# Optimization experiments

Measured on AMD Instinct MI355X. Metric: run time of the kernel, lower is better.

The kernel has to match this reference:

```python
import jax, jax.numpy as jnp
import numpy as np

LN_EPS = 1e-5
N_HEADS = 8

def _ln(x, g, b):
    mu = jnp.mean(x, axis=-1, keepdims=True)
    var = jnp.var(x, axis=-1, keepdims=True)
    return (x - mu) * jax.lax.rsqrt(var + LN_EPS) * g + b

def _glu(x):
    a, b = jnp.split(x, 2, axis=-1)
    return a * jax.nn.sigmoid(b)

def setup_inputs() -> dict:
    key = jax.random.key(0)
    ks = iter(jax.random.split(key, 48))
    B, C, HW, p = 16, 3, 224, 16
    d, N, M = 512, 2048, 25
    Sa, So, O, T = 512, 1024, 1000, 16
    P = (HW // p) ** 2
    rn = lambda shape, s=1.0: jax.random.normal(next(ks), shape, jnp.float32) * s
    inp = {
        'x': rn((B, C, HW, HW)),
        'conv_w': rn((d, C, p, p), 0.02), 'conv_b': jnp.zeros((d,)),
        'patch_ln_g': jnp.ones((d,)), 'patch_ln_b': jnp.zeros((d,)),
        'pos': rn((1, P, d), 0.02),
        'kv_w': rn((d, d), d ** -0.5), 'kv_b': jnp.zeros((d,)),
        'kv_ln_g': jnp.ones((d,)), 'kv_ln_b': jnp.zeros((d,)),
        'q_w': rn((d, Sa), Sa ** -0.5), 'q_b': jnp.zeros((d,)),
        'attn_in_w': rn((3 * d, d), d ** -0.5), 'attn_in_b': jnp.zeros((3 * d,)),
        'attn_out_w': rn((d, d), d ** -0.5), 'attn_out_b': jnp.zeros((d,)),
        'syn_w': rn((2 * N, d + N), (d + N) ** -0.5), 'syn_b': jnp.zeros((2 * N,)),
        'syn_ln_g': jnp.ones((N,)), 'syn_ln_b': jnp.zeros((N,)),
        'fc1_w': rn((N, M, 256), (2.0 / M) ** 0.5), 'fc1_b': jnp.zeros((N, 256)),
        'fc2_w': rn((N, 128, 2), (2.0 / 128) ** 0.5), 'fc2_b': jnp.zeros((N, 2)),
        'nlm_T': jnp.ones((1,)),
        'start_state': rn((N,), (1.0 / N) ** 0.5),
        'start_trace': rn((N, M), (1.0 / (N + M)) ** 0.5),
        'decay_action': jnp.zeros((Sa,)), 'decay_out': jnp.zeros((So,)),
        'out_w': rn((O, So), So ** -0.5), 'out_b': jnp.zeros((O,)),
        'act_left': jax.random.randint(next(ks), (Sa,), 0, N, jnp.int32),
        'act_right': jax.random.randint(next(ks), (Sa,), 0, N, jnp.int32),
        'out_left': jax.random.randint(next(ks), (So,), 0, N, jnp.int32),
        'out_right': jax.random.randint(next(ks), (So,), 0, N, jnp.int32),
        'ticks': T,
    }
    return inp

def _forward(x, conv_w, conv_b, patch_ln_g, patch_ln_b, pos, kv_w, kv_b, kv_ln_g, kv_ln_b,
             q_w, q_b, attn_in_w, attn_in_b, attn_out_w, attn_out_b,
             syn_w, syn_b, syn_ln_g, syn_ln_b, fc1_w, fc1_b, fc2_w, fc2_b, nlm_T,
             start_state, start_trace, decay_action, decay_out, out_w, out_b,
             act_left, act_right, out_left, out_right, ticks):
    B = x.shape[0]
    d = conv_w.shape[0]
    hd = d // N_HEADS
    scale = 1.0 / (hd ** 0.5)
    # --- patch embedding: Conv2d(stride=patch) -> flatten -> LN, then +pos ---
    pt = jax.lax.conv_general_dilated(
        x, conv_w, (conv_w.shape[2], conv_w.shape[3]), 'VALID',
        dimension_numbers=('NCHW', 'OIHW', 'NCHW')) + conv_b[None, :, None, None]
    pt = pt.reshape(B, d, -1).transpose(0, 2, 1)            # (B, P, d)
    pt = _ln(pt, patch_ln_g, patch_ln_b) + pos
    kv = _ln(pt @ kv_w.T + kv_b, kv_ln_g, kv_ln_b)          # (B, P, d)
    wq, wk, wv = jnp.split(attn_in_w, 3)
    bq, bk, bv = jnp.split(attn_in_b, 3)
    k = (kv @ wk.T + bk).reshape(B, -1, N_HEADS, hd)        # (B, P, H, hd)
    v = (kv @ wv.T + bv).reshape(B, -1, N_HEADS, hd)
    r_a = jnp.exp(-decay_action)
    r_o = jnp.exp(-decay_out)

    def sync(act, alpha, beta, r, left, right):
        pair = act[:, left] * act[:, right]                 # (B, S)
        alpha = r * alpha + pair
        beta = r * beta + 1.0
        return alpha * jax.lax.rsqrt(beta), alpha, beta

    def nlm(trace):
        h1 = _glu(jnp.einsum('bnm,nmh->bnh', trace, fc1_w) + fc1_b)  # (B, N, 128)
        h2 = _glu(jnp.einsum('bnh,nho->bno', h1, fc2_w) + fc2_b)     # (B, N, 1)
        return h2[..., 0] / nlm_T[0]

    act0 = jnp.broadcast_to(start_state, (B,) + start_state.shape)
    trace0 = jnp.broadcast_to(start_trace, (B,) + start_trace.shape)
    Sa = act_left.shape[0]
    So = out_left.shape[0]
    _, ao0, bo0 = sync(act0, jnp.zeros((B, So)), jnp.zeros((B, So)), r_o, out_left, out_right)
    carry0 = (trace0, act0, jnp.zeros((B, Sa)), jnp.zeros((B, Sa)), ao0, bo0)

    def step(carry, _):
        trace, act, aa, ba, ao, bo = carry
        s_act, aa, ba = sync(act, aa, ba, r_a, act_left, act_right)
        qv = s_act @ q_w.T + q_b                            # (B, d)
        qh = (qv @ wq.T + bq).reshape(B, N_HEADS, hd) * scale
        attn_w = jax.nn.softmax(jnp.einsum('bhd,bphd->bhp', qh, k), axis=-1)
        attn = jnp.einsum('bhp,bphd->bhd', attn_w, v).reshape(B, d) @ attn_out_w.T + attn_out_b
        pre = jnp.concatenate([attn, act], axis=-1)         # (B, d+N)
        state = _ln(_glu(pre @ syn_w.T + syn_b), syn_ln_g, syn_ln_b)  # (B, N)
        trace = jnp.concatenate([trace[:, :, 1:], state[:, :, None]], axis=-1)
        act = nlm(trace)
        s_out, ao, bo = sync(act, ao, bo, r_o, out_left, out_right)
        pred = s_out @ out_w.T + out_b                      # (B, out_dims)
        return (trace, act, aa, ba, ao, bo), pred

    _, preds = jax.lax.scan(step, carry0, None, length=ticks)
    preds = jnp.moveaxis(preds, 0, -1)                      # (B, out_dims, ticks)
    probs = jax.nn.softmax(preds, axis=1)
    ent = -jnp.sum(probs * jnp.log(probs + 1e-10), axis=1) / jnp.log(float(preds.shape[1]))
    return preds, ent

def reference(x, conv_w, conv_b, patch_ln_g, patch_ln_b, pos, kv_w, kv_b, kv_ln_g, kv_ln_b,
              q_w, q_b, attn_in_w, attn_in_b, attn_out_w, attn_out_b,
              syn_w, syn_b, syn_ln_g, syn_ln_b, fc1_w, fc1_b, fc2_w, fc2_b, nlm_T,
              start_state, start_trace, decay_action, decay_out, out_w, out_b,
              act_left, act_right, out_left, out_right, ticks):
    return _forward(x, conv_w, conv_b, patch_ln_g, patch_ln_b, pos, kv_w, kv_b, kv_ln_g, kv_ln_b,
                    q_w, q_b, attn_in_w, attn_in_b, attn_out_w, attn_out_b,
                    syn_w, syn_b, syn_ln_g, syn_ln_b, fc1_w, fc1_b, fc2_w, fc2_b, nlm_T,
                    start_state, start_trace, decay_action, decay_out, out_w, out_b,
                    act_left, act_right, out_left, out_right, ticks)
```

## Files before the change

kernel.cpp:

```cpp
#include <hip/hip_runtime.h>
#include <hip/hip_bf16.h>
#include <math.h>


#define DEV __device__ __forceinline__
typedef const float* fp;
typedef const float4* f4p;

#define B_   16
#define P_   196
#define D_   512
#define H_   8
#define HD_  64
#define N_   2048
#define M_   25
#define SA_  512
#define SO_  1024
#define O_   1000
#define T_   16

DEV float sigmf(float x){ return 1.0f / (1.0f + expf(-x)); }
DEV float wred(float v) { for (int m = 32; m; m >>= 1) v += __shfl_xor(v, m); return v; }
DEV float f4dot(float4 a, float4 b) { return a.x*b.x + a.y*b.y + a.z*b.z + a.w*b.w; }

DEV float breduce_sum(float v, float* red) {
  int t = threadIdx.x;
  red[t] = v; __syncthreads();
  for (int s = 128; s > 0; s >>= 1) {
    if (t < s) red[t] += red[t + s];
    __syncthreads();
  }
  float r = red[0]; __syncthreads();
  return r;
}
DEV float breduce_max(float v, float* red) {
  int t = threadIdx.x;
  red[t] = v; __syncthreads();
  for (int s = 128; s > 0; s >>= 1) {
    if (t < s) red[t] = fmaxf(red[t], red[t + s]);
    __syncthreads();
  }
  float r = red[0]; __syncthreads();
  return r;
}

__global__ __launch_bounds__(256) void k_patch_tile(fp x, fp conv_w, fp conv_b, float* pt) {
  int i0 = blockIdx.x * 64;
  int j0 = blockIdx.y * 64;
  int tid = threadIdx.x;
  int ti = tid >> 4, tj = tid & 15;
  __shared__ float As[64][20];
  __shared__ float Bs[64][20];
  float acc[4][4] = {{0,0,0,0},{0,0,0,0},{0,0,0,0},{0,0,0,0}};
  int p_loc = tid >> 2, k4 = (tid & 3) * 4;
  int bp = i0 + p_loc;
  int b = bp / P_, p = bp % P_;
  int ph = p / 14, pw = p % 14;
  const float* xbase = x + (size_t)b*3*224*224 + (size_t)(ph*16)*224 + pw*16;
  for (int kc = 0; kc < 48; kc++) {
    int ci = kc >> 4, qi = kc & 15;
    *(float4*)&As[p_loc][k4] = *(f4p)(xbase + ((size_t)ci*224 + qi)*224 + k4);
    *(float4*)&Bs[p_loc][k4] = *(f4p)(conv_w + (size_t)(j0 + p_loc)*768 + kc*16 + k4);
    __syncthreads();
    for (int kk = 0; kk < 16; kk++) {
      float a0 = As[ti*4+0][kk], a1 = As[ti*4+1][kk];
      float a2 = As[ti*4+2][kk], a3 = As[ti*4+3][kk];
      float b0 = Bs[tj*4+0][kk], b1 = Bs[tj*4+1][kk];
      float b2 = Bs[tj*4+2][kk], b3 = Bs[tj*4+3][kk];
      acc[0][0] += a0*b0; acc[0][1] += a0*b1; acc[0][2] += a0*b2; acc[0][3] += a0*b3;
      acc[1][0] += a1*b0; acc[1][1] += a1*b1; acc[1][2] += a1*b2; acc[1][3] += a1*b3;
      acc[2][0] += a2*b0; acc[2][1] += a2*b1; acc[2][2] += a2*b2; acc[2][3] += a2*b3;
      acc[3][0] += a3*b0; acc[3][1] += a3*b1; acc[3][2] += a3*b2; acc[3][3] += a3*b3;
    }
    __syncthreads();
  }
  for (int ii = 0; ii < 4; ii++)
    for (int jj = 0; jj < 4; jj++)
      pt[(size_t)(i0 + ti*4 + ii)*D_ + j0 + tj*4 + jj] = acc[ii][jj] + conv_b[j0 + tj*4 + jj];
}

__global__ __launch_bounds__(256) void k_pln(float* pt, fp g, fp bb, fp pos) {
  int bp0 = blockIdx.x * 16;
  int tid = threadIdx.x, wave = tid >> 6, lane = tid & 63;
  for (int i = 0; i < 4; i++) {
    int bp = bp0 + wave*4 + i;
    int p = bp % P_;
    float* row = pt + (size_t)bp*D_;
    float4 v0 = *(f4p)(row + lane*8);
    float4 v1 = *(f4p)(row + lane*8 + 4);
    float s = v0.x+v0.y+v0.z+v0.w + v1.x+v1.y+v1.z+v1.w;
    float q = f4dot(v0,v0) + f4dot(v1,v1);
    s = wred(s); q = wred(q);
    float mu = s / (float)D_;
    float var = q / (float)D_ - mu*mu;
    float rstd = 1.f / sqrtf(var + 1e-5f);
    for (int j = 0; j < 8; j++) {
      int c = lane*8 + j;
      float v = (j < 4) ? ((const float*)&v0)[j] : ((const float*)&v1)[j-4];
      row[c] = (v - mu)*rstd*g[c] + bb[c] + pos[p*D_ + c];
    }
  }
}

__global__ __launch_bounds__(256) void k_kv_tile(const float* ptin, fp kv_w, fp kv_b, float* kvraw) {
  int i0 = blockIdx.x * 64;
  int j0 = blockIdx.y * 64;
  int tid = threadIdx.x;
  int ti = tid >> 4, tj = tid & 15;
  __shared__ float As[64][20];
  __shared__ float Bs[64][20];
  float acc[4][4] = {{0,0,0,0},{0,0,0,0},{0,0,0,0},{0,0,0,0}};
  int p_loc = tid >> 2, k4 = (tid & 3) * 4;
  for (int kc = 0; kc < 32; kc++) {
    *(float4*)&As[p_loc][k4] = *(f4p)(ptin + (size_t)(i0 + p_loc)*D_ + kc*16 + k4);
    *(float4*)&Bs[p_loc][k4] = *(f4p)(kv_w + (size_t)(j0 + p_loc)*D_ + kc*16 + k4);
    __syncthreads();
    for (int kk = 0; kk < 16; kk++) {
      float a0 = As[ti*4+0][kk], a1 = As[ti*4+1][kk];
      float a2 = As[ti*4+2][kk], a3 = As[ti*4+3][kk];
      float b0 = Bs[tj*4+0][kk], b1 = Bs[tj*4+1][kk];
      float b2 = Bs[tj*4+2][kk], b3 = Bs[tj*4+3][kk];
      acc[0][0] += a0*b0; acc[0][1] += a0*b1; acc[0][2] += a0*b2; acc[0][3] += a0*b3;
      acc[1][0] += a1*b0; acc[1][1] += a1*b1; acc[1][2] += a1*b2; acc[1][3] += a1*b3;
      acc[2][0] += a2*b0; acc[2][1] += a2*b1; acc[2][2] += a2*b2; acc[2][3] += a2*b3;
      acc[3][0] += a3*b0; acc[3][1] += a3*b1; acc[3][2] += a3*b2; acc[3][3] += a3*b3;
    }
    __syncthreads();
  }
  for (int ii = 0; ii < 4; ii++)
    for (int jj = 0; jj < 4; jj++)
      kvraw[(size_t)(i0 + ti*4 + ii)*D_ + j0 + tj*4 + jj] = acc[ii][jj] + kv_b[j0 + tj*4 + jj];
}

__global__ __launch_bounds__(256) void k_kvln(float* kv, fp g, fp bb) {
  int bp0 = blockIdx.x * 16;
  int tid = threadIdx.x, wave = tid >> 6, lane = tid & 63;
  for (int i = 0; i < 4; i++) {
    int bp = bp0 + wave*4 + i;
    float* row = kv + (size_t)bp*D_;
    float4 v0 = *(f4p)(row + lane*8);
    float4 v1 = *(f4p)(row + lane*8 + 4);
    float s = v0.x+v0.y+v0.z+v0.w + v1.x+v1.y+v1.z+v1.w;
    float q = f4dot(v0,v0) + f4dot(v1,v1);
    s = wred(s); q = wred(q);
    float mu = s / (float)D_;
    float var = q / (float)D_ - mu*mu;
    float rstd = 1.f / sqrtf(var + 1e-5f);
    for (int j = 0; j < 8; j++) {
      int c = lane*8 + j;
      float v = (j < 4) ? ((const float*)&v0)[j] : ((const float*)&v1)[j-4];
      row[c] = (v - mu)*rstd*g[c] + bb[c];
    }
  }
}

__global__ __launch_bounds__(256) void k_wqc(fp aw, fp q_w, float* W_qc) {
  int i0 = blockIdx.x * 16, s0 = blockIdx.y * 16;
  int tid = threadIdx.x, il = tid >> 4, sl = tid & 15;
  __shared__ float s_wq[16][129];
  __shared__ float s_qw[128][17];
  float acc = 0.f;
  for (int kc = 0; kc < 4; kc++) {
    int k0 = kc * 128;
    for (int idx = tid; idx < 2048; idx += 256) {
      int r = idx >> 7, c = idx & 127;
      s_wq[r][c] = aw[(size_t)(i0 + r)*512 + k0 + c];
    }
    for (int idx = tid; idx < 2048; idx += 256) {
      int r = idx >> 4, c = idx & 15;
      s_qw[r][c] = q_w[(size_t)(k0 + r)*512 + s0 + c];
    }
    __syncthreads();
    for (int kk = 0; kk < 128; kk++)
      acc += s_wq[il][kk] * s_qw[kk][sl];
    __syncthreads();
  }
  W_qc[(size_t)(i0 + il)*512 + s0 + sl] = 0.125f * acc;
}

__global__ __launch_bounds__(256) void k_wqcb(fp aw, fp q_b, fp ab, float* bc) {
  int i = blockIdx.x * 256 + threadIdx.x;
  float acc = ab[i];
  for (int j = 0; j < 512; j++) acc += aw[(size_t)i*512 + j] * q_b[j];
  bc[i] = 0.125f * acc;
}

__global__ void k_init(fp start_state, fp start_trace, const int* oL, const int* oR,
                       fp decay_a, fp decay_o,
                       float* act, float* trace, float* aaA, float* baA,
                       float* aoA, float* boA, float* r_a, float* r_o) {
  int gid = blockIdx.x * 256 + threadIdx.x;
  if (gid < B_*N_*M_) {
    int bn = gid / M_, m = gid % M_;
    int n = bn % N_;
    trace[gid] = start_trace[n*M_ + m];
  }
  if (gid < B_*N_) act[gid] = start_state[gid & (N_-1)];
  if (gid < B_*SA_) { aaA[gid] = 0.f; baA[gid] = 0.f; }
  if (gid < B_*SO_) {
    int s = gid & (SO_-1);
    aoA[gid] = start_state[oL[s]] * start_state[oR[s]];
    boA[gid] = 1.0f;
  }
  if (gid < SA_) r_a[gid] = expf(-decay_a[gid]);
  if (gid < SO_) r_o[gid] = expf(-decay_o[gid]);
}

__global__ __launch_bounds__(256) void k_attout(
    const float* act,
    float* aaA, float* aaB, float* baA, float* baB,
    float* aoA, float* aoB, float* boA, float* boB,
    const float* r_a, const float* r_o,
    const float* W_qc, const float* bc, const float* kvb,
    fp aw, fp ab, fp out_w, fp out_b,
    const int* aL, const int* aR, const int* oL, const int* oR,
    float* av_ws, float* out, int t) {
  __shared__ float smem[8448];
  int bid = blockIdx.x;
  int tid = threadIdx.x, wave = tid >> 6, lane = tid & 63;

  if (bid < 128) {
    const float* aaR = (t & 1) ? aaB : aaA;  float* aaW = (t & 1) ? aaA : aaB;
    const float* baR = (t & 1) ? baB : baA;  float* baW = (t & 1) ? baA : baB;
    int b = bid >> 3, h = bid & 7;
    float* sact = smem;
    float* qhh  = smem + 512;
    float* qt   = smem + 576;
    float* mW   = smem + 1088;
    float* lW   = smem + 1092;
    float* zzL  = smem + 1600;
    float* zpart= smem + 2112;
    for (int cc = 0; cc < 2; cc++) {
      int s = tid + cc*256;
      float r = r_a[s];
      float pair = act[b*N_ + aL[s]] * act[b*N_ + aR[s]];
      float a  = r*aaR[b*SA_ + s] + pair;
      float bt = r*baR[b*SA_ + s] + 1.0f;
      if (h == 0) { aaW[b*SA_ + s] = a; baW[b*SA_ + s] = bt; }
      sact[s] = a / sqrtf(bt);
    }
    __syncthreads();
    for (int k = 0; k < 16; k++) {
      int r = h*HD_ + wave*16 + k;
      const float* wr = W_qc + (size_t)r*512 + lane*4;
      float s = f4dot(*(f4p)(wr),       *(f4p)(&sact[lane*4]))
              + f4dot(*(f4p)(wr + 256), *(f4p)(&sact[lane*4 + 256]));
      s = wred(s);
      if (lane == 0) qhh[wave*16 + k] = s + bc[r];
    }
    __syncthreads();
    float acc0 = 0.f, acc1 = 0.f;
    for (int e = 0; e < HD_; e++) {
      float q = qhh[e];
      const float* ar = aw + (size_t)(512 + h*HD_ + e)*D_;
      acc0 += q * ar[tid];
      acc1 += q * ar[tid + 256];
    }
    qt[tid] = acc0; qt[tid + 256] = acc1;
    float kb = 0.f;
    for (int e = 0; e < HD_; e++) kb += qhh[e] * ab[512 + h*HD_ + e];
    __syncthreads();
    float qreg[8];
    for (int j = 0; j < 8; j++) qreg[j] = qt[lane*8 + j];
    float m = -1e30f, l = 0.f;
    float zz8[8] = {0,0,0,0,0,0,0,0};
    for (int p = wave*49; p < wave*49 + 49; p++) {
      const float* kvp = kvb + ((size_t)(b*P_ + p))*D_ + lane*8;
      float4 v0 = *(f4p)(kvp), v1 = *(f4p)(kvp + 4);
      float d = v0.x*qreg[0] + v0.y*qreg[1] + v0.z*qreg[2] + v0.w*qreg[3]
              + v1.x*qreg[4] + v1.y*qreg[5] + v1.z*qreg[6] + v1.w*qreg[7];
      d = wred(d);
      float s_p = d + kb;
      float m_new = fmaxf(m, s_p);
      float scale = expf(m - m_new);
      float e = expf(s_p - m_new);
      l = l*scale + e;
      zz8[0] = zz8[0]*scale + e*v0.x; zz8[1] = zz8[1]*scale + e*v0.y;
      zz8[2] = zz8[2]*scale + e*v0.z; zz8[3] = zz8[3]*scale + e*v0.w;
      zz8[4] = zz8[4]*scale + e*v1.x; zz8[5] = zz8[5]*scale + e*v1.y;
      zz8[6] = zz8[6]*scale + e*v1.z; zz8[7] = zz8[7]*scale + e*v1.w;
      m = m_new;
    }
    if (lane == 0) { mW[wave] = m; lW[wave] = l; }
    for (int j = 0; j < 8; j++) zpart[wave*512 + lane*8 + j] = zz8[j];
    __syncthreads();
    {
      float M0 = fmaxf(fmaxf(mW[0], mW[1]), fmaxf(mW[2], mW[3]));
      float f0 = expf(mW[0]-M0), f1 = expf(mW[1]-M0), f2 = expf(mW[2]-M0), f3 = expf(mW[3]-M0);
      float L = lW[0]*f0 + lW[1]*f1 + lW[2]*f2 + lW[3]*f3;
      float invL = 1.f / L;
      for (int cc = 0; cc < 2; cc++) {
        int c = tid + cc*256;
        zzL[c] = (zpart[c]*f0 + zpart[512 + c]*f1 + zpart[1024 + c]*f2 + zpart[1536 + c]*f3) * invL;
      }
    }
    __syncthreads();
    for (int k = 0; k < 16; k++) {
      int e2 = wave*16 + k;
      int r = 1024 + h*HD_ + e2;
      const float* wr = aw + (size_t)r*512 + lane*4;
      float s = f4dot(*(f4p)(wr),       *(f4p)(&zzL[lane*4]))
              + f4dot(*(f4p)(wr + 256), *(f4p)(&zzL[lane*4 + 256]));
      s = wred(s);
      if (lane == 0) av_ws[b*D_ + h*HD_ + e2] = s + ab[r];
    }
  } else if (t > 0) {
    int s_ = t - 1;
    const float* aoR = (s_ & 1) ? aoB : aoA;  float* aoW = (s_ & 1) ? aoA : aoB;
    const float* boR = (s_ & 1) ? boB : boA;  float* boW = (s_ & 1) ? boA : boB;
    int obid = bid - 128;
    int rb = obid >> 1, bg = obid & 1;
    float* s_sout = smem;
    for (int i = 0; i < 32; i++) {
      int idx = tid + i*256;
      int bb = idx >> 10, s = idx & 1023;
      int b = bg*8 + bb;
      float r = r_o[s];
      float pair = act[b*N_ + oL[s]] * act[b*N_ + oR[s]];
      float a  = r*aoR[b*SO_ + s] + pair;
      float bt = r*boR[b*SO_ + s] + 1.f;
      if (rb == 0) { aoW[b*SO_ + s] = a; boW[b*SO_ + s] = bt; }
      s_sout[bb*1024 + s] = a / sqrtf(bt);
    }
    __syncthreads();
    for (int k = 0; k < 5; k++) {
      int r = rb*20 + wave*5 + k;
      const float* wr = out_w + (size_t)r*1024 + lane*4;
      float4 w0 = *(f4p)(wr),       w1 = *(f4p)(wr + 256),
             w2 = *(f4p)(wr + 512), w3 = *(f4p)(wr + 768);
      float pp[8];
      for (int bb = 0; bb < 8; bb++) {
        const float* pb = &s_sout[bb*1024 + lane*4];
        pp[bb] = f4dot(w0, *(f4p)(pb))       + f4dot(w1, *(f4p)(pb + 256))
               + f4dot(w2, *(f4p)(pb + 512)) + f4dot(w3, *(f4p)(pb + 768));
      }
      float obr = out_b[r];
      for (int bb = 0; bb < 8; bb++) {
        float s = wred(pp[bb]);
        if (lane == 0) out[((size_t)((bg*8 + bb)*O_ + r))*T_ + s_] = s + obr;
      }
    }
  }
}

__global__ __launch_bounds__(256) void k_ao2(const float* av_ws, fp ow, fp ob, float* attn_o) {
  int rb = blockIdx.x, bg = blockIdx.y;
  int tid = threadIdx.x, wave = tid >> 6, lane = tid & 63;
  __shared__ float s_a[8][516];
  for (int idx = tid; idx < 8*512; idx += 256) {
    int bb = idx >> 9, c = idx & 511;
    s_a[bb][c] = av_ws[(bg*8 + bb)*D_ + c];
  }
  __syncthreads();
  for (int k = 0; k < 8; k++) {
    int r = rb*32 + wave*8 + k;
    const float* wr = ow + (size_t)r*512 + lane*4;
    float4 w0 = *(f4p)(wr), w1 = *(f4p)(wr + 256);
    float pp[8];
    for (int bb = 0; bb < 8; bb++) {
      const float* pb = &s_a[bb][lane*4];
      pp[bb] = f4dot(w0, *(f4p)(pb)) + f4dot(w1, *(f4p)(pb + 256));
    }
    float obr = ob[r];
    for (int bb = 0; bb < 8; bb++) {
      float s = wred(pp[bb]);
      if (lane == 0) attn_o[(bg*8 + bb)*D_ + r] = s + obr;
    }
  }
}

__global__ __launch_bounds__(256) void k_syn(const float* attn_o, const float* act,
                                             fp syn_w, fp syn_b, float* ysyn,
                                             float* psum, float* psq) {
  int rb = blockIdx.x, bg = blockIdx.y;
  int tid = threadIdx.x, wave = tid >> 6, lane = tid & 63;
  __shared__ float pre8[8*2560];
  __shared__ float wsum[4][8], wsq[4][8];
  for (int bb = 0; bb < 8; bb++) {
    int b = bg*8 + bb;
    for (int i = tid; i < 2560; i += 256)
      pre8[bb*2560 + i] = (i < 512) ? attn_o[b*D_ + i] : act[b*N_ + (i - 512)];
  }
  __syncthreads();
  float lsum[8] = {0,0,0,0,0,0,0,0}, lsq[8] = {0,0,0,0,0,0,0,0};
  for (int k = 0; k < 4; k++) {
    int pr = rb*16 + wave*4 + k;
    float sA[8];
    {
      const float* wr = syn_w + (size_t)pr*2560 + lane*4;
      float4 wreg[10];
      for (int j = 0; j < 10; j++) wreg[j] = *(f4p)(wr + j*256);
      float pp[8] = {0,0,0,0,0,0,0,0};
      for (int j = 0; j < 10; j++) {
        int idx = lane*4 + j*256;
        for (int bb = 0; bb < 8; bb++)
          pp[bb] += f4dot(wreg[j], *(f4p)(&pre8[bb*2560 + idx]));
      }
      float sb = syn_b[pr];
      for (int bb = 0; bb < 8; bb++) sA[bb] = wred(pp[bb]) + sb;
    }
    {
      int r2 = pr + 2048;
      const float* wr = syn_w + (size_t)r2*2560 + lane*4;
      float4 wreg[10];
      for (int j = 0; j < 10; j++) wreg[j] = *(f4p)(wr + j*256);
      float pp[8] = {0,0,0,0,0,0,0,0};
      for (int j = 0; j < 10; j++) {
        int idx = lane*4 + j*256;
        for (int bb = 0; bb < 8; bb++)
          pp[bb] += f4dot(wreg[j], *(f4p)(&pre8[bb*2560 + idx]));
      }
      float sb = syn_b[r2];
      for (int bb = 0; bb < 8; bb++) {
        float sG = wred(pp[bb]) + sb;
        float v = sA[bb] * sigmf(sG);
        lsum[bb] += v; lsq[bb] += v*v;
        if (lane == 0) ysyn[(size_t)(bg*8 + bb)*N_ + pr] = v;
      }
    }
  }
  if (lane == 0)
    for (int bb = 0; bb < 8; bb++) { wsum[wave][bb] = lsum[bb]; wsq[wave][bb] = lsq[bb]; }
  __syncthreads();
  if (tid < 8) {
    float s1 = wsum[0][tid] + wsum[1][tid] + wsum[2][tid] + wsum[3][tid];
    float s2 = wsq[0][tid]  + wsq[1][tid]  + wsq[2][tid]  + wsq[3][tid];
    psum[rb*16 + bg*8 + tid] = s1;
    psq [rb*16 + bg*8 + tid] = s2;
  }
}

__global__ __launch_bounds__(256) void k_nlm(float* trace, const float* ysyn,
                                             const float* psum, const float* psq,
                                             fp sg, fp sb2,
                                             fp fc1_w, fp fc1_b, fp fc2_w, fp fc2_b,
                                             fp nlmT, float* act) {
  int n = blockIdx.x, tid = threadIdx.x;
  __shared__ float tr[B_][M_];
  __shared__ float uu[256][17];
  __shared__ float h1[128][17];
  __shared__ float vout[B_][2];
  __shared__ float s_mu[16], s_rstd[16];
  {
    int b = tid >> 4, j = tid & 15;
    float s1 = 0.f, s2 = 0.f;
    for (int rb = j; rb < 128; rb += 16) { s1 += psum[rb*16 + b]; s2 += psq[rb*16 + b]; }
    for (int m = 8; m; m >>= 1) { s1 += __shfl_xor(s1, m); s2 += __shfl_xor(s2, m); }
    if (j == 0) {
      float mu = s1 / (float)N_;
      s_mu[b] = mu;
      s_rstd[b] = 1.f / sqrtf(s2 / (float)N_ - mu*mu + 1e-5f);
    }
  }
  __syncthreads();
  for (int i = tid; i < B_*M_; i += 256) {
    int b = i / M_, m = i % M_;
    float v;
    if (m < M_-1) v = trace[((size_t)(b*N_ + n))*M_ + m + 1];
    else          v = (ysyn[(size_t)b*N_ + n] - s_mu[b]) * s_rstd[b] * sg[n] + sb2[n];
    tr[b][m] = v;
  }
  __syncthreads();
  for (int i = tid; i < B_*M_; i += 256) {
    int b = i / M_, m = i % M_;
    trace[((size_t)(b*N_ + n))*M_ + m] = tr[b][m];
  }
  float w25[M_];
  for (int m = 0; m < M_; m++) w25[m] = fc1_w[((size_t)n*M_ + m)*256 + tid];
  float bias = fc1_b[n*256 + tid];
  for (int b = 0; b < B_; b++) {
    float u = bias;
    for (int m = 0; m < M_; m++) u += tr[b][m]*w25[m];
    uu[tid][b] = u;
  }
  __syncthreads();
  if (tid < 128) {
    for (int b = 0; b < B_; b++)
      h1[tid][b] = uu[tid][b] * sigmf(uu[tid + 128][b]);
  }
  __syncthreads();
  {
    int b = tid >> 4, o = (tid >> 3) & 1, part = tid & 7;
    const float* f2 = fc2_w + (size_t)n*256;
    float acc = 0.f;
    for (int i = 0; i < 16; i++) {
      int hh = part*16 + i;
      acc += h1[hh][b] * f2[hh*2 + o];
    }
    for (int m2 = 4; m2; m2 >>= 1) acc += __shfl_xor(acc, m2);
    if (part == 0) vout[b][o] = acc + fc2_b[n*2 + o];
  }
  __syncthreads();
  if (tid < B_) {
    act[tid*N_ + n] = vout[tid][0] * sigmf(vout[tid][1]) / nlmT[0];
  }
}

__global__ __launch_bounds__(256) void k_out(const float* act, const float* aoR, const float* boR,
                                             float* aoW, float* boW, const float* r_o,
                                             const int* L, const int* R,
                                             fp out_w, fp out_b, float* out, int t) {
  int rb = blockIdx.x, bg = blockIdx.y;
  int tid = threadIdx.x, wave = tid >> 6, lane = tid & 63;
  __shared__ float s_sout[8][1024];
  for (int i = 0; i < 32; i++) {
    int idx = tid + i*256;
    int bb = idx >> 10, s = idx & 1023;
    int b = bg*8 + bb;
    float r = r_o[s];
    float pair = act[b*N_ + L[s]] * act[b*N_ + R[s]];
    float a  = r*aoR[b*SO_ + s] + pair;
    float bt = r*boR[b*SO_ + s] + 1.f;
    if (rb == 0) { aoW[b*SO_ + s] = a; boW[b*SO_ + s] = bt; }
    s_sout[bb][s] = a / sqrtf(bt);
  }
  __syncthreads();
  for (int k = 0; k < 5; k++) {
    int r = rb*20 + wave*5 + k;
    const float* wr = out_w + (size_t)r*1024 + lane*4;
    float4 w0 = *(f4p)(wr),       w1 = *(f4p)(wr + 256),
           w2 = *(f4p)(wr + 512), w3 = *(f4p)(wr + 768);
    float pp[8];
    for (int bb = 0; bb < 8; bb++) {
      const float* pb = &s_sout[bb][lane*4];
      pp[bb] = f4dot(w0, *(f4p)(pb))       + f4dot(w1, *(f4p)(pb + 256))
             + f4dot(w2, *(f4p)(pb + 512)) + f4dot(w3, *(f4p)(pb + 768));
    }
    float obr = out_b[r];
    for (int bb = 0; bb < 8; bb++) {
      float s = wred(pp[bb]);
      if (lane == 0) out[((size_t)((bg*8 + bb)*O_ + r))*T_ + t] = s + obr;
    }
  }
}

__global__ __launch_bounds__(256) void k_final(float* out) {
  int b = blockIdx.x, t = blockIdx.y, tid = threadIdx.x;
  __shared__ float red[256];
  float lm = -1e30f;
  for (int o = tid; o < O_; o += 256) lm = fmaxf(lm, out[((size_t)(b*O_ + o))*T_ + t]);
  float Mx = breduce_max(lm, red);
  float le = 0.f;
  for (int o = tid; o < O_; o += 256) le += expf(out[((size_t)(b*O_ + o))*T_ + t] - Mx);
  float S = breduce_sum(le, red);
  float lt = 0.f;
  for (int o = tid; o < O_; o += 256) {
    float pr = expf(out[((size_t)(b*O_ + o))*T_ + t] - Mx) / S;
    lt += pr * logf(pr + 1e-10f);
  }
  float E = breduce_sum(lt, red);
  if (tid == 0)
    out[(size_t)B_*O_*T_ + b*T_ + t] = -E / logf((float)O_);
}

extern "C" void kernel_launch(void* const* d_in, const int* in_sizes, int n_in,
                              void* d_out, int out_size, void* d_ws, size_t ws_size,
                              hipStream_t stream) {
  (void)in_sizes; (void)n_in; (void)out_size; (void)ws_size;
  fp x          = (fp)d_in[0];
  fp conv_w     = (fp)d_in[1];
  fp conv_b     = (fp)d_in[2];
  fp patch_ln_g = (fp)d_in[3];
  fp patch_ln_b = (fp)d_in[4];
  fp pos        = (fp)d_in[5];
  fp kv_w       = (fp)d_in[6];
  fp kv_b       = (fp)d_in[7];
  fp kv_ln_g    = (fp)d_in[8];
  fp kv_ln_b    = (fp)d_in[9];
  fp q_w        = (fp)d_in[10];
  fp q_b        = (fp)d_in[11];
  fp attn_in_w  = (fp)d_in[12];
  fp attn_in_b  = (fp)d_in[13];
  fp attn_out_w = (fp)d_in[14];
  fp attn_out_b = (fp)d_in[15];
  fp syn_w      = (fp)d_in[16];
  fp syn_b      = (fp)d_in[17];
  fp syn_ln_g   = (fp)d_in[18];
  fp syn_ln_b   = (fp)d_in[19];
  fp fc1_w      = (fp)d_in[20];
  fp fc1_b      = (fp)d_in[21];
  fp fc2_w      = (fp)d_in[22];
  fp fc2_b      = (fp)d_in[23];
  fp nlm_T      = (fp)d_in[24];
  fp start_state= (fp)d_in[25];
  fp start_trace= (fp)d_in[26];
  fp decay_a    = (fp)d_in[27];
  fp decay_o    = (fp)d_in[28];
  fp out_w      = (fp)d_in[29];
  fp out_b      = (fp)d_in[30];
  const int* act_left  = (const int*)d_in[31];
  const int* act_right = (const int*)d_in[32];
  const int* out_left  = (const int*)d_in[33];
  const int* out_right = (const int*)d_in[34];

  float* ws = (float*)d_ws;
  float* pt     = ws;
  float* act    = ws + 0;
  float* trace  = ws + 32768;
  float* aaA    = ws + 851968;
  float* aaB    = ws + 860160;
  float* baA    = ws + 868352;
  float* baB    = ws + 876544;
  float* aoA    = ws + 884736;
  float* aoB    = ws + 901120;
  float* boA    = ws + 917504;
  float* boB    = ws + 933888;
  float* attn_o = ws + 958464;
  float* ysyn   = ws + 966656;
  float* psum   = ws + 999424;
  float* psq    = ws + 1001472;
  float* av_ws  = ws + 1064960;
  float* r_a    = ws + 1073152;
  float* r_o    = ws + 1073664;
  float* W_qc   = ws + 1074688;
  float* bc     = ws + 1336832;
  float* kvb    = ws + 1605632;

  k_patch_tile<<<dim3(49, 8), dim3(256), 0, stream>>>(x, conv_w, conv_b, pt);
  k_pln<<<dim3(196), dim3(256), 0, stream>>>(pt, patch_ln_g, patch_ln_b, pos);
  k_kv_tile<<<dim3(49, 8), dim3(256), 0, stream>>>(pt, kv_w, kv_b, kvb);
  k_kvln<<<dim3(196), dim3(256), 0, stream>>>(kvb, kv_ln_g, kv_ln_b);
  k_wqc<<<dim3(32, 32), dim3(256), 0, stream>>>(attn_in_w, q_w, W_qc);
  k_wqcb<<<dim3(2), dim3(256), 0, stream>>>(attn_in_w, q_b, attn_in_b, bc);
  k_init<<<dim3((B_*N_*M_ + 255)/256), dim3(256), 0, stream>>>(start_state, start_trace,
        out_left, out_right, decay_a, decay_o, act, trace, aaA, baA, aoA, boA, r_a, r_o);

  for (int t = 0; t < T_; t++) {
    k_attout<<<dim3(228), dim3(256), 0, stream>>>(
        act, aaA, aaB, baA, baB, aoA, aoB, boA, boB, r_a, r_o,
        W_qc, bc, kvb, attn_in_w, attn_in_b, out_w, out_b,
        act_left, act_right, out_left, out_right, av_ws, (float*)d_out, t);
    k_ao2<<<dim3(16, 2), dim3(256), 0, stream>>>(av_ws, attn_out_w, attn_out_b, attn_o);
    k_syn<<<dim3(128, 2), dim3(256), 0, stream>>>(attn_o, act, syn_w, syn_b, ysyn, psum, psq);
    k_nlm<<<dim3(N_), dim3(256), 0, stream>>>(trace, ysyn, psum, psq, syn_ln_g, syn_ln_b,
                                              fc1_w, fc1_b, fc2_w, fc2_b, nlm_T, act);
  }
  {
    int t = T_ - 1;
    const float* aoR = (t & 1) ? aoB : aoA;  float* aoW = (t & 1) ? aoA : aoB;
    const float* boR = (t & 1) ? boB : boA;  float* boW = (t & 1) ? boA : boB;
    k_out<<<dim3(50, 2), dim3(256), 0, stream>>>(act, aoR, boR, aoW, boW, r_o,
                                                 out_left, out_right, out_w, out_b,
                                                 (float*)d_out, t);
  }
  k_final<<<dim3(16, 16), dim3(256), 0, stream>>>((float*)d_out);
}
```

Measured before the change: 3.005 ms.

## Fold attention output projection into synapse weights and transpose GEMM B tiles

Precomputes W_so = syn_w[:, :512] @ attn_out_w and a folded bias once before the tick loop. Each tick then runs one fused synapse kernel directly on the attention values, dropping the separate attention-output projection launch. The fused path is used only when the workspace is large enough, otherwise the old path runs. Separately, the shared-memory B tiles in the conv and kv GEMMs are stored transposed so each inner-loop step reads them with one float4 load. The cost is an extra precompute GEMM, about 8 MB of extra workspace, and a change in float rounding order.

```diff
diff --git a/kernel.cpp b/kernel.cpp
--- a/kernel.cpp
+++ b/kernel.cpp
@@ -50,7 +50,7 @@
   int tid = threadIdx.x;
   int ti = tid >> 4, tj = tid & 15;
   __shared__ float As[64][20];
-  __shared__ float Bs[64][20];
+  __shared__ float Bsx[16][68];
   float acc[4][4] = {{0,0,0,0},{0,0,0,0},{0,0,0,0},{0,0,0,0}};
   int p_loc = tid >> 2, k4 = (tid & 3) * 4;
   int bp = i0 + p_loc;
@@ -60,17 +60,18 @@
   for (int kc = 0; kc < 48; kc++) {
     int ci = kc >> 4, qi = kc & 15;
     *(float4*)&As[p_loc][k4] = *(f4p)(xbase + ((size_t)ci*224 + qi)*224 + k4);
-    *(float4*)&Bs[p_loc][k4] = *(f4p)(conv_w + (size_t)(j0 + p_loc)*768 + kc*16 + k4);
+    float4 bv = *(f4p)(conv_w + (size_t)(j0 + p_loc)*768 + kc*16 + k4);
+    Bsx[k4+0][p_loc] = bv.x; Bsx[k4+1][p_loc] = bv.y;
+    Bsx[k4+2][p_loc] = bv.z; Bsx[k4+3][p_loc] = bv.w;
     __syncthreads();
     for (int kk = 0; kk < 16; kk++) {
       float a0 = As[ti*4+0][kk], a1 = As[ti*4+1][kk];
       float a2 = As[ti*4+2][kk], a3 = As[ti*4+3][kk];
-      float b0 = Bs[tj*4+0][kk], b1 = Bs[tj*4+1][kk];
-      float b2 = Bs[tj*4+2][kk], b3 = Bs[tj*4+3][kk];
-      acc[0][0] += a0*b0; acc[0][1] += a0*b1; acc[0][2] += a0*b2; acc[0][3] += a0*b3;
-      acc[1][0] += a1*b0; acc[1][1] += a1*b1; acc[1][2] += a1*b2; acc[1][3] += a1*b3;
-      acc[2][0] += a2*b0; acc[2][1] += a2*b1; acc[2][2] += a2*b2; acc[2][3] += a2*b3;
-      acc[3][0] += a3*b0; acc[3][1] += a3*b1; acc[3][2] += a3*b2; acc[3][3] += a3*b3;
+      float4 bq = *(f4p)&Bsx[kk][tj*4];
+      acc[0][0] += a0*bq.x; acc[0][1] += a0*bq.y; acc[0][2] += a0*bq.z; acc[0][3] += a0*bq.w;
+      acc[1][0] += a1*bq.x; acc[1][1] += a1*bq.y; acc[1][2] += a1*bq.z; acc[1][3] += a1*bq.w;
+      acc[2][0] += a2*bq.x; acc[2][1] += a2*bq.y; acc[2][2] += a2*bq.z; acc[2][3] += a2*bq.w;
+      acc[3][0] += a3*bq.x; acc[3][1] += a3*bq.y; acc[3][2] += a3*bq.z; acc[3][3] += a3*bq.w;
     }
     __syncthreads();
   }
@@ -108,22 +109,23 @@
   int tid = threadIdx.x;
   int ti = tid >> 4, tj = tid & 15;
   __shared__ float As[64][20];
-  __shared__ float Bs[64][20];
+  __shared__ float Bsx[16][68];
   float acc[4][4] = {{0,0,0,0},{0,0,0,0},{0,0,0,0},{0,0,0,0}};
   int p_loc = tid >> 2, k4 = (tid & 3) * 4;
   for (int kc = 0; kc < 32; kc++) {
     *(float4*)&As[p_loc][k4] = *(f4p)(ptin + (size_t)(i0 + p_loc)*D_ + kc*16 + k4);
-    *(float4*)&Bs[p_loc][k4] = *(f4p)(kv_w + (size_t)(j0 + p_loc)*D_ + kc*16 + k4);
+    float4 bv = *(f4p)(kv_w + (size_t)(j0 + p_loc)*D_ + kc*16 + k4);
+    Bsx[k4+0][p_loc] = bv.x; Bsx[k4+1][p_loc] = bv.y;
+    Bsx[k4+2][p_loc] = bv.z; Bsx[k4+3][p_loc] = bv.w;
     __syncthreads();
     for (int kk = 0; kk < 16; kk++) {
       float a0 = As[ti*4+0][kk], a1 = As[ti*4+1][kk];
       float a2 = As[ti*4+2][kk], a3 = As[ti*4+3][kk];
-      float b0 = Bs[tj*4+0][kk], b1 = Bs[tj*4+1][kk];
-      float b2 = Bs[tj*4+2][kk], b3 = Bs[tj*4+3][kk];
-      acc[0][0] += a0*b0; acc[0][1] += a0*b1; acc[0][2] += a0*b2; acc[0][3] += a0*b3;
-      acc[1][0] += a1*b0; acc[1][1] += a1*b1; acc[1][2] += a1*b2; acc[1][3] += a1*b3;
-      acc[2][0] += a2*b0; acc[2][1] += a2*b1; acc[2][2] += a2*b2; acc[2][3] += a2*b3;
-      acc[3][0] += a3*b0; acc[3][1] += a3*b1; acc[3][2] += a3*b2; acc[3][3] += a3*b3;
+      float4 bq = *(f4p)&Bsx[kk][tj*4];
+      acc[0][0] += a0*bq.x; acc[0][1] += a0*bq.y; acc[0][2] += a0*bq.z; acc[0][3] += a0*bq.w;
+      acc[1][0] += a1*bq.x; acc[1][1] += a1*bq.y; acc[1][2] += a1*bq.z; acc[1][3] += a1*bq.w;
+      acc[2][0] += a2*bq.x; acc[2][1] += a2*bq.y; acc[2][2] += a2*bq.z; acc[2][3] += a2*bq.w;
+      acc[3][0] += a3*bq.x; acc[3][1] += a3*bq.y; acc[3][2] += a3*bq.z; acc[3][3] += a3*bq.w;
     }
     __syncthreads();
   }
@@ -183,6 +185,44 @@
   float acc = ab[i];
   for (int j = 0; j < 512; j++) acc += aw[(size_t)i*512 + j] * q_b[j];
   bc[i] = 0.125f * acc;
+}
+
+__global__ __launch_bounds__(256) void k_wso(fp syn_w, fp ow, float* W_so) {
+  int i0 = blockIdx.x * 64;
+  int j0 = blockIdx.y * 64;
+  int tid = threadIdx.x;
+  int ti = tid >> 4, tj = tid & 15;
+  __shared__ float As[64][20];
+  __shared__ float Bsx[16][68];
+  float acc[4][4] = {{0,0,0,0},{0,0,0,0},{0,0,0,0},{0,0,0,0}};
+  int p_loc = tid >> 2, k4 = (tid & 3) * 4;
+  int kr = tid >> 4, c4 = (tid & 15) * 4;
+  for (int kc = 0; kc < 32; kc++) {
+    *(float4*)&As[p_loc][k4] = *(f4p)(syn_w + (size_t)(i0 + p_loc)*2560 + kc*16 + k4);
+    *(float4*)&Bsx[kr][c4]   = *(f4p)(ow + (size_t)(kc*16 + kr)*512 + j0 + c4);
+    __syncthreads();
+    for (int kk = 0; kk < 16; kk++) {
+      float a0 = As[ti*4+0][kk], a1 = As[ti*4+1][kk];
+      float a2 = As[ti*4+2][kk], a3 = As[ti*4+3][kk];
+      float4 bq = *(f4p)&Bsx[kk][tj*4];
+      acc[0][0] += a0*bq.x; acc[0][1] += a0*bq.y; acc[0][2] += a0*bq.z; acc[0][3] += a0*bq.w;
+      acc[1][0] += a1*bq.x; acc[1][1] += a1*bq.y; acc[1][2] += a1*bq.z; acc[1][3] += a1*bq.w;
+      acc[2][0] += a2*bq.x; acc[2][1] += a2*bq.y; acc[2][2] += a2*bq.z; acc[2][3] += a2*bq.w;
+      acc[3][0] += a3*bq.x; acc[3][1] += a3*bq.y; acc[3][2] += a3*bq.z; acc[3][3] += a3*bq.w;
+    }
+    __syncthreads();
+  }
+  for (int ii = 0; ii < 4; ii++)
+    for (int jj = 0; jj < 4; jj++)
+      W_so[(size_t)(i0 + ti*4 + ii)*512 + j0 + tj*4 + jj] = acc[ii][jj];
+}
+
+__global__ __launch_bounds__(256) void k_wsob(fp syn_w, fp syn_b, fp ob, float* syn_b2) {
+  int r = blockIdx.x * 256 + threadIdx.x;
+  float acc = syn_b[r];
+  const float* wr = syn_w + (size_t)r*2560;
+  for (int j = 0; j < 512; j++) acc += wr[j] * ob[j];
+  syn_b2[r] = acc;
 }
 
 __global__ void k_init(fp start_state, fp start_trace, const int* oL, const int* oR,
@@ -369,6 +409,71 @@
   }
 }
 
+__global__ __launch_bounds__(256) void k_syn2(const float* av_ws, const float* act,
+                                              const float* W_so, fp syn_w, const float* syn_b2,
+                                              float* ysyn, float* psum, float* psq) {
+  int rb = blockIdx.x, bg = blockIdx.y;
+  int tid = threadIdx.x, wave = tid >> 6, lane = tid & 63;
+  __shared__ float pre8[8*2560];
+  __shared__ float wsum[4][8], wsq[4][8];
+  for (int bb = 0; bb < 8; bb++) {
+    int b = bg*8 + bb;
+    for (int i = tid; i < 2560; i += 256)
+      pre8[bb*2560 + i] = (i < 512) ? av_ws[b*D_ + i] : act[b*N_ + (i - 512)];
+  }
+  __syncthreads();
+  float lsum[8] = {0,0,0,0,0,0,0,0}, lsq[8] = {0,0,0,0,0,0,0,0};
+  for (int k = 0; k < 4; k++) {
+    int pr = rb*16 + wave*4 + k;
+    float sA[8];
+    {
+      float4 wreg[10];
+      wreg[0] = *(f4p)(W_so + (size_t)pr*512 + lane*4);
+      wreg[1] = *(f4p)(W_so + (size_t)pr*512 + 256 + lane*4);
+      for (int j = 2; j < 10; j++)
+        wreg[j] = *(f4p)(syn_w + (size_t)pr*2560 + 512 + (j-2)*256 + lane*4);
+      float pp[8] = {0,0,0,0,0,0,0,0};
+      for (int j = 0; j < 10; j++) {
+        int idx = lane*4 + j*256;
+        for (int bb = 0; bb < 8; bb++)
+          pp[bb] += f4dot(wreg[j], *(f4p)(&pre8[bb*2560 + idx]));
+      }
+      float sb = syn_b2[pr];
+      for (int bb = 0; bb < 8; bb++) sA[bb] = wred(pp[bb]) + sb;
+    }
+    {
+      int r2 = pr + 2048;
+      float4 wreg[10];
+      wreg[0] = *(f4p)(W_so + (size_t)r2*512 + lane*4);
+      wreg[1] = *(f4p)(W_so + (size_t)r2*512 + 256 + lane*4);
+      for (int j = 2; j < 10; j++)
+        wreg[j] = *(f4p)(syn_w + (size_t)r2*2560 + 512 + (j-2)*256 + lane*4);
+      float pp[8] = {0,0,0,0,0,0,0,0};
+      for (int j = 0; j < 10; j++) {
+        int idx = lane*4 + j*256;
+        for (int bb = 0; bb < 8; bb++)
+          pp[bb] += f4dot(wreg[j], *(f4p)(&pre8[bb*2560 + idx]));
+      }
+      float sb = syn_b2[r2];
+      for (int bb = 0; bb < 8; bb++) {
+        float sG = wred(pp[bb]) + sb;
+        float v = sA[bb] * sigmf(sG);
+        lsum[bb] += v; lsq[bb] += v*v;
+        if (lane == 0) ysyn[(size_t)(bg*8 + bb)*N_ + pr] = v;
+      }
+    }
+  }
+  if (lane == 0)
+    for (int bb = 0; bb < 8; bb++) { wsum[wave][bb] = lsum[bb]; wsq[wave][bb] = lsq[bb]; }
+  __syncthreads();
+  if (tid < 8) {
+    float s1 = wsum[0][tid] + wsum[1][tid] + wsum[2][tid] + wsum[3][tid];
+    float s2 = wsq[0][tid]  + wsq[1][tid]  + wsq[2][tid]  + wsq[3][tid];
+    psum[rb*16 + bg*8 + tid] = s1;
+    psq [rb*16 + bg*8 + tid] = s2;
+  }
+}
+
 __global__ __launch_bounds__(256) void k_syn(const float* attn_o, const float* act,
                                              fp syn_w, fp syn_b, float* ysyn,
                                              float* psum, float* psq) {
@@ -556,7 +661,7 @@
 extern "C" void kernel_launch(void* const* d_in, const int* in_sizes, int n_in,
                               void* d_out, int out_size, void* d_ws, size_t ws_size,
                               hipStream_t stream) {
-  (void)in_sizes; (void)n_in; (void)out_size; (void)ws_size;
+  (void)in_sizes; (void)n_in; (void)out_size;
   fp x          = (fp)d_in[0];
   fp conv_w     = (fp)d_in[1];
   fp conv_b     = (fp)d_in[2];
@@ -615,6 +720,9 @@
   float* W_qc   = ws + 1074688;
   float* bc     = ws + 1336832;
   float* kvb    = ws + 1605632;
+  float* W_so   = ws + 3211264;
+  float* syn_b2 = ws + 5308416;
+  const bool big = ws_size >= (size_t)5312512 * 4;
 
   k_patch_tile<<<dim3(49, 8), dim3(256), 0, stream>>>(x, conv_w, conv_b, pt);
   k_pln<<<dim3(196), dim3(256), 0, stream>>>(pt, patch_ln_g, patch_ln_b, pos);
@@ -622,6 +730,10 @@
   k_kvln<<<dim3(196), dim3(256), 0, stream>>>(kvb, kv_ln_g, kv_ln_b);
   k_wqc<<<dim3(32, 32), dim3(256), 0, stream>>>(attn_in_w, q_w, W_qc);
   k_wqcb<<<dim3(2), dim3(256), 0, stream>>>(attn_in_w, q_b, attn_in_b, bc);
+  if (big) {
+    k_wso<<<dim3(64, 8), dim3(256), 0, stream>>>(syn_w, attn_out_w, W_so);
+    k_wsob<<<dim3(16), dim3(256), 0, stream>>>(syn_w, syn_b, attn_out_b, syn_b2);
+  }
   k_init<<<dim3((B_*N_*M_ + 255)/256), dim3(256), 0, stream>>>(start_state, start_trace,
         out_left, out_right, decay_a, decay_o, act, trace, aaA, baA, aoA, boA, r_a, r_o);
 
@@ -630,8 +742,13 @@
         act, aaA, aaB, baA, baB, aoA, aoB, boA, boB, r_a, r_o,
         W_qc, bc, kvb, attn_in_w, attn_in_b, out_w, out_b,
         act_left, act_right, out_left, out_right, av_ws, (float*)d_out, t);
-    k_ao2<<<dim3(16, 2), dim3(256), 0, stream>>>(av_ws, attn_out_w, attn_out_b, attn_o);
-    k_syn<<<dim3(128, 2), dim3(256), 0, stream>>>(attn_o, act, syn_w, syn_b, ysyn, psum, psq);
+    if (big) {
+      k_syn2<<<dim3(128, 2), dim3(256), 0, stream>>>(av_ws, act, W_so, syn_w, syn_b2,
+                                                     ysyn, psum, psq);
+    } else {
+      k_ao2<<<dim3(16, 2), dim3(256), 0, stream>>>(av_ws, attn_out_w, attn_out_b, attn_o);
+      k_syn<<<dim3(128, 2), dim3(256), 0, stream>>>(attn_o, act, syn_w, syn_b, ysyn, psum, psq);
+    }
     k_nlm<<<dim3(N_), dim3(256), 0, stream>>>(trace, ysyn, psum, psq, syn_ln_g, syn_ln_b,
                                               fc1_w, fc1_b, fc2_w, fc2_b, nlm_T, act);
   }
```

Result: faster. 2.834 ms (-5.7%).
